# Optimization experiments

Hardware: AMD Instinct MI355X
Metric: run time of the kernel (lower is better)

## Reference

```python
import jax, jax.numpy as jnp
import numpy as np


def setup_inputs() -> dict:
    key = jax.random.key(0)
    k1, k2 = jax.random.split(key)
    N, M, C = 8192, 16384, 128
    features = jax.random.normal(k1, (N, 1, 1, C), dtype=jnp.float32)
    patch_memory = jax.random.normal(k2, (1, M, 1, C), dtype=jnp.float32)
    return {"features": features, "patch_memory": patch_memory}


def reference(features, patch_memory):
    # Faithful to: torch.norm(features - patch_memory, dim=3); torch.min(dim=1)
    # features: [N, 1, 1, C], patch_memory: [1, M, 1, C] -> broadcast diff [N, M, 1, C]
    # Avoid materializing the [N, M, C] diff tensor: use the GEMM expansion
    # ||a-b||^2 = ||a||^2 + ||b||^2 - 2 a.b (same math, efficient form).
    f = features.reshape(features.shape[0], features.shape[-1])       # [N, C]
    m = patch_memory.reshape(patch_memory.shape[1], patch_memory.shape[-1])  # [M, C]
    f2 = jnp.sum(f * f, axis=-1)   # [N]
    m2 = jnp.sum(m * m, axis=-1)   # [M]
    cross = jnp.einsum('nc,mc->nm', f, m)  # [N, M]
    d2 = f2[:, None] + m2[None, :] - 2.0 * cross
    distances = jnp.sqrt(jnp.maximum(d2, 0.0))       # [N, M] == norm over dim 3
    min_distances = jnp.min(distances, axis=1)       # min over memory dim (dim=1)
    # original keeps the trailing singleton patch dim -> [N, 1]
    return min_distances[:, None]
```

## Files before the change

### kernel.cpp

```cpp
#include <hip/hip_runtime.h>
#include <hip/hip_bf16.h>
#include <stdint.h>

#define N_ROWS 8192
#define M_ROWS 16384
#define CDIM 128
#define NT 32
#define BROWS 64

typedef unsigned short u16;
typedef __attribute__((ext_vector_type(2))) unsigned short u16x2;
typedef __attribute__((ext_vector_type(8))) short bf16x8;
typedef __attribute__((ext_vector_type(4))) float f32x4;

static __device__ __forceinline__ u16 f2bf(float x) {
  union { float f; uint32_t u; } v; v.f = x;
  uint32_t u = v.u;
  uint32_t r = u + 0x7FFFu + ((u >> 16) & 1u);
  return (u16)(r >> 16);
}
static __device__ __forceinline__ float bf2f(u16 b) {
  union { uint32_t u; float f; } v; v.u = ((uint32_t)b) << 16;
  return v.f;
}

__global__ __launch_bounds__(256) void prep_kernel(
    const float* __restrict__ f, const float* __restrict__ m,
    u16* __restrict__ fb, u16* __restrict__ mb,
    float* __restrict__ f2, float* __restrict__ mh, int* __restrict__ mind2)
{
  const int row = blockIdx.x * 4 + (threadIdx.x >> 6);
  const int lane = threadIdx.x & 63;
  const bool isF = row < N_ROWS;
  const float* src = isF ? (f + (size_t)row * CDIM)
                         : (m + (size_t)(row - N_ROWS) * CDIM);
  float2 v = *(const float2*)(src + lane * 2);
  u16 b0 = f2bf(v.x), b1 = f2bf(v.y);
  float x0 = bf2f(b0), x1 = bf2f(b1);
  float s = x0 * x0 + x1 * x1;
#pragma unroll
  for (int mask = 1; mask < 64; mask <<= 1)
    s += __shfl_xor(s, mask, 64);
  u16x2 bb = {b0, b1};
  if (isF) {
    *(u16x2*)(fb + (size_t)row * CDIM + lane * 2) = bb;
    if (lane == 0) { f2[row] = s; mind2[row] = 0x7F7FFFFF; }
  } else {
    const int r = row - N_ROWS;
    *(u16x2*)(mb + (size_t)r * CDIM + lane * 2) = bb;
    if (lane == 0) mh[r] = -0.5f * s;
  }
}

__global__ __launch_bounds__(256, 2) void gemm_min_kernel(
    const u16* __restrict__ fb, const u16* __restrict__ mb,
    const float* __restrict__ f2, const float* __restrict__ mh,
    int* __restrict__ mind2)
{
  __shared__ __align__(16) u16 bts[2][BROWS * CDIM];
  __shared__ __align__(16) float mhl[2048];
  const int tid = threadIdx.x;
  const int msplit = blockIdx.x;
  const int nbase = blockIdx.y * 128;

  const int lane = tid & 63;
  const int w = tid >> 6;
  const int wr = w >> 1, wc = w & 1;
  const int l15 = lane & 15, l4 = lane >> 4;
  const int sw = (l15 & 7) << 4;

  int srcOffs[4], dstOffs[4];
#pragma unroll
  for (int c = 0; c < 4; ++c) {
    const int t16 = c * 256 + tid;
    srcOffs[c] = (t16 ^ ((t16 >> 4) & 7)) * 8;
    dstOffs[c] = t16 * 8;
  }

  {
    const u16* srcA = fb + (size_t)nbase * CDIM;
    u16* base = &bts[0][0];
#pragma unroll
    for (int c = 0; c < 8; ++c) {
      const int t16 = c * 256 + tid;
      const int so = (t16 ^ ((t16 >> 4) & 7)) * 8;
      __builtin_amdgcn_global_load_lds(
          (const __attribute__((address_space(1))) uint32_t*)(srcA + so),
          (__attribute__((address_space(3))) uint32_t*)(base + t16 * 8), 16, 0, 0);
    }
    const float* srcM = mh + msplit * 2048;
#pragma unroll
    for (int c = 0; c < 2; ++c) {
      const int c16 = c * 256 + tid;
      __builtin_amdgcn_global_load_lds(
          (const __attribute__((address_space(1))) uint32_t*)(srcM + c16 * 4),
          (__attribute__((address_space(3))) uint32_t*)(&mhl[c16 * 4]), 16, 0, 0);
    }
  }
  asm volatile("s_waitcnt vmcnt(0)" ::: "memory");
  __builtin_amdgcn_s_barrier();

  bf16x8 af[4][4];
  {
    const u16* base = &bts[0][0];
#pragma unroll
    for (int mi = 0; mi < 4; ++mi)
#pragma unroll
      for (int ks = 0; ks < 4; ++ks) {
        const int row = wr * 64 + mi * 16 + l15;
        const int cb = (ks * 64 + l4 * 16) ^ sw;
        af[mi][ks] = *(const bf16x8*)&base[row * CDIM + (cb >> 1)];
      }
  }
  __syncthreads();

  {
    const u16* srcB = mb + (size_t)(msplit * 2048) * CDIM;
    u16* dstB = &bts[0][0];
#pragma unroll
    for (int c = 0; c < 4; ++c)
      __builtin_amdgcn_global_load_lds(
          (const __attribute__((address_space(1))) uint32_t*)(srcB + srcOffs[c]),
          (__attribute__((address_space(3))) uint32_t*)(dstB + dstOffs[c]), 16, 0, 0);
  }

  float tmax[4][4];
#pragma unroll
  for (int mi = 0; mi < 4; ++mi)
#pragma unroll
    for (int j = 0; j < 4; ++j) tmax[mi][j] = -3.0e38f;

  for (int t = 0; t < NT; ++t) {
    __builtin_amdgcn_s_barrier();
    asm volatile("" ::: "memory");
    {
      const int tn = (t + 1) & (NT - 1);
      const u16* srcB = mb + (size_t)(msplit * 2048 + tn * BROWS) * CDIM;
      u16* dstB = &bts[(t + 1) & 1][0];
#pragma unroll
      for (int c = 0; c < 4; ++c)
        __builtin_amdgcn_global_load_lds(
            (const __attribute__((address_space(1))) uint32_t*)(srcB + srcOffs[c]),
            (__attribute__((address_space(3))) uint32_t*)(dstB + dstOffs[c]), 16, 0, 0);
    }
    asm volatile("s_waitcnt vmcnt(4)" ::: "memory");

    const u16* bt = &bts[t & 1][0];
    const int brow0 = wc * 32 + l15;
    const float mh0 = mhl[t * BROWS + brow0];
    const float mh1 = mhl[t * BROWS + brow0 + 16];

    f32x4 acc[4][2];
#pragma unroll
    for (int mi = 0; mi < 4; ++mi) {
      acc[mi][0] = (f32x4){mh0, mh0, mh0, mh0};
      acc[mi][1] = (f32x4){mh1, mh1, mh1, mh1};
    }

    __builtin_amdgcn_s_setprio(1);
#pragma unroll
    for (int ks = 0; ks < 4; ++ks) {
      const int cb = (ks * 64 + l4 * 16) ^ sw;
      const bf16x8 bg0 = *(const bf16x8*)&bt[brow0 * CDIM + (cb >> 1)];
      const bf16x8 bg1 = *(const bf16x8*)&bt[(brow0 + 16) * CDIM + (cb >> 1)];
#pragma unroll
      for (int mi = 0; mi < 4; ++mi) {
        acc[mi][0] = __builtin_amdgcn_mfma_f32_16x16x32_bf16(
            af[mi][ks], bg0, acc[mi][0], 0, 0, 0);
        acc[mi][1] = __builtin_amdgcn_mfma_f32_16x16x32_bf16(
            af[mi][ks], bg1, acc[mi][1], 0, 0, 0);
      }
    }
    __builtin_amdgcn_s_setprio(0);

#pragma unroll
    for (int mi = 0; mi < 4; ++mi)
#pragma unroll
      for (int j = 0; j < 4; ++j)
        tmax[mi][j] = fmaxf(tmax[mi][j], fmaxf(acc[mi][0][j], acc[mi][1][j]));
  }

#pragma unroll
  for (int mi = 0; mi < 4; ++mi)
#pragma unroll
    for (int j = 0; j < 4; ++j) {
      float tv = tmax[mi][j];
      tv = fmaxf(tv, __shfl_xor(tv, 1, 64));
      tv = fmaxf(tv, __shfl_xor(tv, 2, 64));
      tv = fmaxf(tv, __shfl_xor(tv, 4, 64));
      tv = fmaxf(tv, __shfl_xor(tv, 8, 64));
      tmax[mi][j] = tv;
    }
  if (l15 == 0) {
#pragma unroll
    for (int mi = 0; mi < 4; ++mi)
#pragma unroll
      for (int j = 0; j < 4; ++j) {
        const int row = nbase + wr * 64 + mi * 16 + l4 * 4 + j;
        const float d2 = fmaxf(fmaf(-2.0f, tmax[mi][j], f2[row]), 0.0f);
        atomicMin(&mind2[row], __float_as_int(d2));
      }
  }
}

__global__ __launch_bounds__(256) void finalize_kernel(
    const int* __restrict__ mind2, float* __restrict__ out)
{
  const int i = blockIdx.x * 256 + threadIdx.x;
  out[i] = sqrtf(fmaxf(__int_as_float(mind2[i]), 0.0f));
}

extern "C" void kernel_launch(void* const* d_in, const int* in_sizes, int n_in,
                              void* d_out, int out_size, void* d_ws, size_t ws_size,
                              hipStream_t stream) {
  const float* f = (const float*)d_in[0];
  const float* m = (const float*)d_in[1];

  char* ws = (char*)d_ws;
  u16*  fb    = (u16*)(ws);
  u16*  mb    = (u16*)(ws + (2u << 20));
  float* f2   = (float*)(ws + (2u << 20) + (4u << 20));
  float* mh   = (float*)(ws + (2u << 20) + (4u << 20) + (32u << 10));
  int*  mind2 = (int*)(ws + (2u << 20) + (4u << 20) + (96u << 10));

  hipLaunchKernelGGL(prep_kernel, dim3((N_ROWS + M_ROWS) / 4), dim3(256), 0, stream,
                     f, m, fb, mb, f2, mh, mind2);
  hipLaunchKernelGGL(gemm_min_kernel, dim3(8, N_ROWS / 128), dim3(256), 0, stream,
                     fb, mb, f2, mh, mind2);
  hipLaunchKernelGGL(finalize_kernel, dim3(N_ROWS / 256), dim3(256), 0, stream,
                     mind2, (float*)d_out);
}
```

Baseline: 48.88 us.

## Enlarge GEMM-min tiles to 256x128 with triple-buffered, phase-interleaved B loads

The fused distance-GEMM/min kernel now uses 512-thread blocks covering 256 feature rows and 128-row memory tiles. B tiles go through a three-stage LDS ring filled two tiles ahead, and each tile is split into four phases that interleave the async global-to-LDS loads, the LDS reads and the MFMAs, with sched_barriers and one block barrier per phase. The goal is to hide load latency and cut barriers per MFMA. The cost is more LDS per block (about 104 KB), which may limit occupancy to one block per CU, plus more barriers per tile.

```diff
diff --git a/kernel.cpp b/kernel.cpp
--- a/kernel.cpp
+++ b/kernel.cpp
@@ -5,8 +5,8 @@
 #define N_ROWS 8192
 #define M_ROWS 16384
 #define CDIM 128
-#define NT 32
-#define BROWS 64
+#define NTILE 16
+#define BTROWS 128
 
 typedef unsigned short u16;
 typedef __attribute__((ext_vector_type(2))) unsigned short u16x2;
@@ -23,6 +23,11 @@
   union { uint32_t u; float f; } v; v.u = ((uint32_t)b) << 16;
   return v.f;
 }
+
+#define GLOAD_LDS(gsrc, ldst)                                                  \
+  __builtin_amdgcn_global_load_lds(                                            \
+      (const __attribute__((address_space(1))) uint32_t*)(gsrc),               \
+      (__attribute__((address_space(3))) uint32_t*)(ldst), 16, 0, 0)
 
 __global__ __launch_bounds__(256) void prep_kernel(
     const float* __restrict__ f, const float* __restrict__ m,
@@ -52,133 +57,128 @@
   }
 }
 
-__global__ __launch_bounds__(256, 2) void gemm_min_kernel(
+__global__ __launch_bounds__(512, 2) void gemm_min_kernel(
     const u16* __restrict__ fb, const u16* __restrict__ mb,
     const float* __restrict__ f2, const float* __restrict__ mh,
     int* __restrict__ mind2)
 {
-  __shared__ __align__(16) u16 bts[2][BROWS * CDIM];
+  __shared__ __align__(16) u16 bts[3 * BTROWS * CDIM];
   __shared__ __align__(16) float mhl[2048];
   const int tid = threadIdx.x;
   const int msplit = blockIdx.x;
-  const int nbase = blockIdx.y * 128;
+  const int nbase = blockIdx.y * 256;
 
   const int lane = tid & 63;
   const int w = tid >> 6;
-  const int wr = w >> 1, wc = w & 1;
+  const int wm = w >> 1;
+  const int wn = w & 1;
   const int l15 = lane & 15, l4 = lane >> 4;
   const int sw = (l15 & 7) << 4;
 
-  int srcOffs[4], dstOffs[4];
-#pragma unroll
-  for (int c = 0; c < 4; ++c) {
-    const int t16 = c * 256 + tid;
-    srcOffs[c] = (t16 ^ ((t16 >> 4) & 7)) * 8;
-    dstOffs[c] = t16 * 8;
-  }
-
   {
     const u16* srcA = fb + (size_t)nbase * CDIM;
-    u16* base = &bts[0][0];
 #pragma unroll
     for (int c = 0; c < 8; ++c) {
-      const int t16 = c * 256 + tid;
+      const int t16 = c * 512 + tid;
       const int so = (t16 ^ ((t16 >> 4) & 7)) * 8;
-      __builtin_amdgcn_global_load_lds(
-          (const __attribute__((address_space(1))) uint32_t*)(srcA + so),
-          (__attribute__((address_space(3))) uint32_t*)(base + t16 * 8), 16, 0, 0);
-    }
-    const float* srcM = mh + msplit * 2048;
-#pragma unroll
-    for (int c = 0; c < 2; ++c) {
-      const int c16 = c * 256 + tid;
-      __builtin_amdgcn_global_load_lds(
-          (const __attribute__((address_space(1))) uint32_t*)(srcM + c16 * 4),
-          (__attribute__((address_space(3))) uint32_t*)(&mhl[c16 * 4]), 16, 0, 0);
-    }
+      GLOAD_LDS(srcA + so, bts + t16 * 8);
+    }
+    GLOAD_LDS(mh + msplit * 2048 + tid * 4, mhl + tid * 4);
   }
   asm volatile("s_waitcnt vmcnt(0)" ::: "memory");
   __builtin_amdgcn_s_barrier();
 
   bf16x8 af[4][4];
-  {
-    const u16* base = &bts[0][0];
+#pragma unroll
+  for (int mi = 0; mi < 4; ++mi)
+#pragma unroll
+    for (int ks = 0; ks < 4; ++ks) {
+      const int row = wm * 64 + mi * 16 + l15;
+      const int cb = (ks * 64 + l4 * 16) ^ sw;
+      af[mi][ks] = *(const bf16x8*)&bts[row * CDIM + (cb >> 1)];
+    }
+  __syncthreads();
+
+  const u16* mbase_ptr = mb + (size_t)(msplit * 2048) * CDIM;
+#pragma unroll
+  for (int tt = 0; tt < 2; ++tt)
+#pragma unroll
+    for (int c = 0; c < 4; ++c) {
+      const int t16 = c * 512 + tid;
+      const int so = (t16 ^ ((t16 >> 4) & 7)) * 8;
+      GLOAD_LDS(mbase_ptr + (size_t)tt * BTROWS * CDIM + so,
+                bts + tt * BTROWS * CDIM + t16 * 8);
+    }
+  asm volatile("s_waitcnt vmcnt(4)" ::: "memory");
+  __builtin_amdgcn_s_barrier();
+
+  float tmax[4][4];
+#pragma unroll
+  for (int mi = 0; mi < 4; ++mi)
+#pragma unroll
+    for (int j = 0; j < 4; ++j) tmax[mi][j] = -3.0e38f;
+
+  f32x4 acc[4][4];
+  int cur = 0;
+
+  for (int t = 0; t < NTILE; ++t) {
+    const u16* bt = bts + cur * BTROWS * CDIM;
+    int stg = cur + 2; if (stg >= 3) stg -= 3;
+    u16* stgbuf = bts + stg * BTROWS * CDIM;
+    const u16* srcT2 = mbase_ptr + (size_t)((t + 2) & (NTILE - 1)) * BTROWS * CDIM;
+
+#pragma unroll
+    for (int p = 0; p < 4; ++p) {
+      if (t) {
+#pragma unroll
+        for (int mi = 0; mi < 4; ++mi)
+#pragma unroll
+          for (int j = 0; j < 4; ++j)
+            tmax[mi][j] = fmaxf(tmax[mi][j], acc[mi][p][j]);
+      }
+      const float mhv = mhl[t * BTROWS + wn * 64 + p * 16 + l15];
+#pragma unroll
+      for (int mi = 0; mi < 4; ++mi)
+        acc[mi][p] = (f32x4){mhv, mhv, mhv, mhv};
+
+      bf16x8 bg[4];
+      {
+        const int row = wn * 64 + p * 16 + l15;
+#pragma unroll
+        for (int ks = 0; ks < 4; ++ks) {
+          const int cb = (ks * 64 + l4 * 16) ^ sw;
+          bg[ks] = *(const bf16x8*)&bt[row * CDIM + (cb >> 1)];
+        }
+      }
+      {
+        const int t16 = p * 512 + tid;
+        const int so = (t16 ^ ((t16 >> 4) & 7)) * 8;
+        GLOAD_LDS(srcT2 + so, stgbuf + t16 * 8);
+      }
+      if (p == 3)
+        asm volatile("s_waitcnt vmcnt(4)" ::: "memory");
+      __builtin_amdgcn_s_barrier();
+      __builtin_amdgcn_sched_barrier(0);
+      __builtin_amdgcn_s_setprio(1);
+#pragma unroll
+      for (int ks = 0; ks < 4; ++ks)
+#pragma unroll
+        for (int mi = 0; mi < 4; ++mi)
+          acc[mi][p] = __builtin_amdgcn_mfma_f32_16x16x32_bf16(
+              af[mi][ks], bg[ks], acc[mi][p], 0, 0, 0);
+      __builtin_amdgcn_s_setprio(0);
+      __builtin_amdgcn_sched_barrier(0);
+    }
+    cur += 1; if (cur >= 3) cur -= 3;
+  }
+
+#pragma unroll
+  for (int p = 0; p < 4; ++p)
 #pragma unroll
     for (int mi = 0; mi < 4; ++mi)
 #pragma unroll
-      for (int ks = 0; ks < 4; ++ks) {
-        const int row = wr * 64 + mi * 16 + l15;
-        const int cb = (ks * 64 + l4 * 16) ^ sw;
-        af[mi][ks] = *(const bf16x8*)&base[row * CDIM + (cb >> 1)];
-      }
-  }
-  __syncthreads();
-
-  {
-    const u16* srcB = mb + (size_t)(msplit * 2048) * CDIM;
-    u16* dstB = &bts[0][0];
-#pragma unroll
-    for (int c = 0; c < 4; ++c)
-      __builtin_amdgcn_global_load_lds(
-          (const __attribute__((address_space(1))) uint32_t*)(srcB + srcOffs[c]),
-          (__attribute__((address_space(3))) uint32_t*)(dstB + dstOffs[c]), 16, 0, 0);
-  }
-
-  float tmax[4][4];
-#pragma unroll
-  for (int mi = 0; mi < 4; ++mi)
-#pragma unroll
-    for (int j = 0; j < 4; ++j) tmax[mi][j] = -3.0e38f;
-
-  for (int t = 0; t < NT; ++t) {
-    __builtin_amdgcn_s_barrier();
-    asm volatile("" ::: "memory");
-    {
-      const int tn = (t + 1) & (NT - 1);
-      const u16* srcB = mb + (size_t)(msplit * 2048 + tn * BROWS) * CDIM;
-      u16* dstB = &bts[(t + 1) & 1][0];
-#pragma unroll
-      for (int c = 0; c < 4; ++c)
-        __builtin_amdgcn_global_load_lds(
-            (const __attribute__((address_space(1))) uint32_t*)(srcB + srcOffs[c]),
-            (__attribute__((address_space(3))) uint32_t*)(dstB + dstOffs[c]), 16, 0, 0);
-    }
-    asm volatile("s_waitcnt vmcnt(4)" ::: "memory");
-
-    const u16* bt = &bts[t & 1][0];
-    const int brow0 = wc * 32 + l15;
-    const float mh0 = mhl[t * BROWS + brow0];
-    const float mh1 = mhl[t * BROWS + brow0 + 16];
-
-    f32x4 acc[4][2];
-#pragma unroll
-    for (int mi = 0; mi < 4; ++mi) {
-      acc[mi][0] = (f32x4){mh0, mh0, mh0, mh0};
-      acc[mi][1] = (f32x4){mh1, mh1, mh1, mh1};
-    }
-
-    __builtin_amdgcn_s_setprio(1);
-#pragma unroll
-    for (int ks = 0; ks < 4; ++ks) {
-      const int cb = (ks * 64 + l4 * 16) ^ sw;
-      const bf16x8 bg0 = *(const bf16x8*)&bt[brow0 * CDIM + (cb >> 1)];
-      const bf16x8 bg1 = *(const bf16x8*)&bt[(brow0 + 16) * CDIM + (cb >> 1)];
-#pragma unroll
-      for (int mi = 0; mi < 4; ++mi) {
-        acc[mi][0] = __builtin_amdgcn_mfma_f32_16x16x32_bf16(
-            af[mi][ks], bg0, acc[mi][0], 0, 0, 0);
-        acc[mi][1] = __builtin_amdgcn_mfma_f32_16x16x32_bf16(
-            af[mi][ks], bg1, acc[mi][1], 0, 0, 0);
-      }
-    }
-    __builtin_amdgcn_s_setprio(0);
-
-#pragma unroll
-    for (int mi = 0; mi < 4; ++mi)
-#pragma unroll
       for (int j = 0; j < 4; ++j)
-        tmax[mi][j] = fmaxf(tmax[mi][j], fmaxf(acc[mi][0][j], acc[mi][1][j]));
-  }
+        tmax[mi][j] = fmaxf(tmax[mi][j], acc[mi][p][j]);
 
 #pragma unroll
   for (int mi = 0; mi < 4; ++mi)
@@ -196,7 +196,7 @@
     for (int mi = 0; mi < 4; ++mi)
 #pragma unroll
       for (int j = 0; j < 4; ++j) {
-        const int row = nbase + wr * 64 + mi * 16 + l4 * 4 + j;
+        const int row = nbase + wm * 64 + mi * 16 + l4 * 4 + j;
         const float d2 = fmaxf(fmaf(-2.0f, tmax[mi][j], f2[row]), 0.0f);
         atomicMin(&mind2[row], __float_as_int(d2));
       }
@@ -225,7 +225,7 @@
 
   hipLaunchKernelGGL(prep_kernel, dim3((N_ROWS + M_ROWS) / 4), dim3(256), 0, stream,
                      f, m, fb, mb, f2, mh, mind2);
-  hipLaunchKernelGGL(gemm_min_kernel, dim3(8, N_ROWS / 128), dim3(256), 0, stream,
+  hipLaunchKernelGGL(gemm_min_kernel, dim3(8, N_ROWS / 256), dim3(512), 0, stream,
                      fb, mb, f2, mh, mind2);
   hipLaunchKernelGGL(finalize_kernel, dim3(N_ROWS / 256), dim3(256), 0, stream,
                      mind2, (float*)d_out);
```

Result: faster. 46.20 us (-5.5%).
